# Performance work log

Hardware: AMD Instinct MI355X
Metric: run time of the kernel (lower is better)

Reference implementation:

```python
import jax, jax.numpy as jnp
import numpy as np

N_WORD, N_DOC, E = 20000, 20000, 500000
H, O, D = 4, 32, 128  # heads, out per head, hidden*heads
NEG_SLOPE = 0.2


def setup_inputs() -> dict:
    key = jax.random.key(0)
    ks = jax.random.split(key, 24)
    rn = lambda k, s, sc=0.1: jax.random.normal(k, s, dtype=jnp.float32) * sc
    ri = lambda k, s, hi: jax.random.randint(k, s, 0, hi, dtype=jnp.int32)
    return {
        'x_word': rn(ks[0], (N_WORD, 300), 1.0),
        'x_doc': rn(ks[1], (N_DOC, D), 1.0),
        'Wp_word': rn(ks[2], (300, D)), 'bp_word': jnp.zeros((D,), jnp.float32),
        'Wp_doc': rn(ks[3], (D, D)), 'bp_doc': jnp.zeros((D,), jnp.float32),
        'Wsrc': rn(ks[4], (2, 3, D, D)), 'bsrc': jnp.zeros((2, 3, D), jnp.float32),
        'Wdst': rn(ks[5], (2, 3, D, D)), 'bdst': jnp.zeros((2, 3, D), jnp.float32),
        'attn': rn(ks[6], (2, 3, H, O)), 'bconv': jnp.zeros((2, 3, D), jnp.float32),
        'Wc1': rn(ks[7], (D, 64)), 'bc1': jnp.zeros((64,), jnp.float32),
        'Wc2': rn(ks[8], (64, 64)), 'bc2': jnp.zeros((64,), jnp.float32),
        'src_wd': ri(ks[9], (E,), N_WORD), 'dst_wd': ri(ks[10], (E,), N_DOC),
        'src_dw': ri(ks[11], (E,), N_DOC), 'dst_dw': ri(ks[12], (E,), N_WORD),
        'src_dd': ri(ks[13], (E,), N_DOC), 'dst_dd': ri(ks[14], (E,), N_DOC),
    }


def _gatv2(h_src, h_dst, src, dst, Ws, bs, Wd, bd, a, bias, n_dst):
    # GATv2Conv (DGL): e = a . leaky_relu(Ws h_u + Wd h_v); edge softmax per dst; sum alpha*Ws h_u
    fs = (h_src @ Ws + bs).reshape(-1, H, O)           # [N_src,H,O]
    fd = (h_dst @ Wd + bd).reshape(-1, H, O)           # [N_dst,H,O]
    e = jax.nn.leaky_relu(fs[src] + fd[dst], NEG_SLOPE)  # [E,H,O]
    score = jnp.einsum('eho,ho->eh', e, a)             # [E,H]
    m = jax.lax.stop_gradient(jax.ops.segment_max(score, dst, num_segments=n_dst))
    ex = jnp.exp(score - m[dst])
    s = jax.ops.segment_sum(ex, dst, num_segments=n_dst)
    alpha = ex / s[dst]                                 # per-dst softmax
    rst = jax.ops.segment_sum(alpha[:, :, None] * fs[src], dst, num_segments=n_dst)
    return rst + bias.reshape(1, H, O)


def reference(x_word, x_doc, Wp_word, bp_word, Wp_doc, bp_doc, Wsrc, bsrc, Wdst, bdst,
              attn, bconv, Wc1, bc1, Wc2, bc2, src_wd, dst_wd, src_dw, dst_dw, src_dd, dst_dd):
    h_w = x_word @ Wp_word + bp_word
    h_d = x_doc @ Wp_doc + bp_doc
    for l in range(2):
        o_wd = _gatv2(h_w, h_d, src_wd, dst_wd, Wsrc[l, 0], bsrc[l, 0], Wdst[l, 0], bdst[l, 0], attn[l, 0], bconv[l, 0], N_DOC)
        o_dw = _gatv2(h_d, h_w, src_dw, dst_dw, Wsrc[l, 1], bsrc[l, 1], Wdst[l, 1], bdst[l, 1], attn[l, 1], bconv[l, 1], N_WORD)
        o_dd = _gatv2(h_d, h_d, src_dd, dst_dd, Wsrc[l, 2], bsrc[l, 2], Wdst[l, 2], bdst[l, 2], attn[l, 2], bconv[l, 2], N_DOC)
        h_d = ((o_wd + o_dd) * 0.5).reshape(N_DOC, D)   # mean over 2 relations into 'document'
        h_w = o_dw.reshape(N_WORD, D)                    # mean over 1 relation into 'word'
    z = jax.nn.relu(h_d @ Wc1 + bc1)
    return z @ Wc2 + bc2  # [N_DOC, len_label]
```

## Files before the change

### kernel.cpp

```cpp
#include <hip/hip_runtime.h>

#define NNODE 20000
#define NEDGE 500000
#define CAP 64
#define RCHUNK 2048
#define NRANGE 8
#define RSZ 2500
#define SCAP 70000
#define XW 64

typedef __attribute__((ext_vector_type(8))) short bf16x8;
typedef __attribute__((ext_vector_type(8))) unsigned short u16x8;
typedef __attribute__((ext_vector_type(4))) float f32x4;

__device__ __forceinline__ unsigned short f2bf(float f) {
    unsigned u = __float_as_uint(f);
    return (unsigned short)((u + 0x7FFFu + ((u >> 16) & 1u)) >> 16);
}
__device__ __forceinline__ float bf2f(unsigned short h) {
    return __uint_as_float((unsigned)h << 16);
}

__device__ __forceinline__ void split_one(
    const float* __restrict__ B, unsigned short* __restrict__ Bt,
    int K, int N, int Kp, int i)
{
    int n = i / Kp, k = i % Kp;
    float v = (k < K) ? B[(size_t)k * N + n] : 0.f;
    unsigned short h = f2bf(v);
    Bt[i] = h;
    Bt[(size_t)N * Kp + i] = f2bf(v - bf2f(h));
}

__device__ __forceinline__ void split_row4(
    const float* __restrict__ X, unsigned short* __restrict__ A2,
    int K, int Kp, int r, int c)
{
    float v[4];
#pragma unroll
    for (int j = 0; j < 4; ++j) v[j] = (c + j < K) ? X[(size_t)r * K + c + j] : 0.f;
    ushort4 hi, lo;
    unsigned short h;
    h = f2bf(v[0]); hi.x = h; lo.x = f2bf(v[0] - bf2f(h));
    h = f2bf(v[1]); hi.y = h; lo.y = f2bf(v[1] - bf2f(h));
    h = f2bf(v[2]); hi.z = h; lo.z = f2bf(v[2] - bf2f(h));
    h = f2bf(v[3]); hi.w = h; lo.w = f2bf(v[3] - bf2f(h));
    *reinterpret_cast<ushort4*>(A2 + (size_t)r * 2 * Kp + c) = hi;
    *reinterpret_cast<ushort4*>(A2 + (size_t)r * 2 * Kp + Kp + c) = lo;
}

__global__ __launch_bounds__(256) void prep_all_kernel(
    const float* __restrict__ Wp_word, const float* __restrict__ Wp_doc,
    const float* __restrict__ Wsrc, const float* __restrict__ Wdst,
    const float* __restrict__ Wc1, const float* __restrict__ Wc2,
    const float* __restrict__ xw, const float* __restrict__ xd,
    unsigned short* __restrict__ WtPw, unsigned short* __restrict__ WtPd,
    unsigned short* __restrict__ WtCat,
    unsigned short* __restrict__ WtC1, unsigned short* __restrict__ WtC2,
    unsigned short* __restrict__ Ax, unsigned short* __restrict__ Axd)
{
    int i = blockIdx.x * 256 + threadIdx.x;
    const int S0 = 128 * 320, S1 = 128 * 128, S2 = 6 * 256 * 128;
    const int S3 = 64 * 128, S4 = 64 * 64;
    const int X1 = NNODE * 80, X2 = NNODE * 32;
    if (i < S0) { split_one(Wp_word, WtPw, 300, 128, 320, i); return; }
    i -= S0;
    if (i < S1) { split_one(Wp_doc, WtPd, 128, 128, 128, i); return; }
    i -= S1;
    if (i < S2) {
        int lc = i / (256 * 128), rem = i % (256 * 128);
        int n = rem / 128, k = rem % 128;
        int l = lc / 3, c = lc % 3;
        int half = n >> 7, nn = n & 127;
        const float* M;
        if (c == 0)      M = half ? (Wdst + (size_t)(l * 3 + 1) * 16384) : (Wsrc + (size_t)(l * 3 + 0) * 16384);
        else if (c == 1) M = half ? (Wsrc + (size_t)(l * 3 + 1) * 16384) : (Wdst + (size_t)(l * 3 + 0) * 16384);
        else             M = half ? (Wdst + (size_t)(l * 3 + 2) * 16384) : (Wsrc + (size_t)(l * 3 + 2) * 16384);
        float v = M[(size_t)k * 128 + nn];
        unsigned short h = f2bf(v);
        unsigned short* Bt = WtCat + (size_t)lc * 65536;
        Bt[(size_t)n * 128 + k] = h;
        Bt[32768 + (size_t)n * 128 + k] = f2bf(v - bf2f(h));
        return;
    }
    i -= S2;
    if (i < S3) { split_one(Wc1, WtC1, 128, 64, 128, i); return; }
    i -= S3;
    if (i < S4) { split_one(Wc2, WtC2, 64, 64, 64, i); return; }
    i -= S4;
    if (i < X1) {
        int r = i / 80, c = (i % 80) * 4;
        split_row4(xw, Ax, 300, 320, r, c);
        return;
    }
    i -= X1;
    if (i < X2) {
        int r = i / 32, c = (i % 32) * 4;
        split_row4(xd, Axd, 128, 128, r, c);
    }
}

template<int BM, int BN, int MODE>
__global__ __launch_bounds__(512) void gemm_mfma_kernel(
    const unsigned short* __restrict__ A2,
    const unsigned short* __restrict__ Bt,
    const float* __restrict__ b0,
    float* __restrict__ C0, unsigned short* __restrict__ S0,
    int M, int Kp, int do_relu)
{
    constexpr int FM = BM / 32;
    constexpr int FN = BN / 64;
    __shared__ unsigned short As[2][BM][40];
    __shared__ unsigned short Bs[2][BN][40];
    const int tid = threadIdx.x;
    const int m0 = blockIdx.x * BM;
    const int wid = tid >> 6, lane = tid & 63;
    const int wm = wid >> 2, wn = wid & 3;
    const int lr = lane & 15, kg = lane >> 4;

    f32x4 acc[FM][FN] = {};
    const size_t KA = 2 * (size_t)Kp;
    const size_t PB = (size_t)BN * Kp;

    for (int k0 = 0; k0 < Kp; k0 += 32) {
#pragma unroll
        for (int idx = tid; idx < BM * 4; idx += 512) {
            int row = idx >> 2, ck = idx & 3;
            u16x8 hi = {0,0,0,0,0,0,0,0}, lo = {0,0,0,0,0,0,0,0};
            if (m0 + row < M) {
                const unsigned short* ap = A2 + (size_t)(m0 + row) * KA + k0 + ck * 8;
                hi = *reinterpret_cast<const u16x8*>(ap);
                lo = *reinterpret_cast<const u16x8*>(ap + Kp);
            }
            *reinterpret_cast<u16x8*>(&As[0][row][ck * 8]) = hi;
            *reinterpret_cast<u16x8*>(&As[1][row][ck * 8]) = lo;
        }
#pragma unroll
        for (int idx = tid; idx < BN * 4; idx += 512) {
            int nr = idx >> 2, ck = idx & 3;
            const unsigned short* bp = Bt + (size_t)nr * Kp + k0 + ck * 8;
            *reinterpret_cast<u16x8*>(&Bs[0][nr][ck * 8]) = *reinterpret_cast<const u16x8*>(bp);
            *reinterpret_cast<u16x8*>(&Bs[1][nr][ck * 8]) = *reinterpret_cast<const u16x8*>(bp + PB);
        }
        __syncthreads();
        bf16x8 ah[FM], al[FM], bh[FN], bl[FN];
#pragma unroll
        for (int fm = 0; fm < FM; ++fm) {
            ah[fm] = *reinterpret_cast<const bf16x8*>(&As[0][wm * (BM / 2) + fm * 16 + lr][kg * 8]);
            al[fm] = *reinterpret_cast<const bf16x8*>(&As[1][wm * (BM / 2) + fm * 16 + lr][kg * 8]);
        }
#pragma unroll
        for (int fn = 0; fn < FN; ++fn) {
            bh[fn] = *reinterpret_cast<const bf16x8*>(&Bs[0][wn * (BN / 4) + fn * 16 + lr][kg * 8]);
            bl[fn] = *reinterpret_cast<const bf16x8*>(&Bs[1][wn * (BN / 4) + fn * 16 + lr][kg * 8]);
        }
#pragma unroll
        for (int fm = 0; fm < FM; ++fm)
#pragma unroll
            for (int fn = 0; fn < FN; ++fn) {
                acc[fm][fn] = __builtin_amdgcn_mfma_f32_16x16x32_bf16(ah[fm], bh[fn], acc[fm][fn], 0, 0, 0);
                acc[fm][fn] = __builtin_amdgcn_mfma_f32_16x16x32_bf16(al[fm], bh[fn], acc[fm][fn], 0, 0, 0);
                acc[fm][fn] = __builtin_amdgcn_mfma_f32_16x16x32_bf16(ah[fm], bl[fn], acc[fm][fn], 0, 0, 0);
            }
        __syncthreads();
    }
#pragma unroll
    for (int fm = 0; fm < FM; ++fm)
#pragma unroll
        for (int fn = 0; fn < FN; ++fn) {
            int gc = wn * (BN / 4) + fn * 16 + lr;
            float bv = b0[gc];
#pragma unroll
            for (int j = 0; j < 4; ++j) {
                int gr = m0 + wm * (BM / 2) + fm * 16 + kg * 4 + j;
                if (gr < M) {
                    float v = acc[fm][fn][j] + bv;
                    if (do_relu) v = fmaxf(v, 0.f);
                    if (MODE == 0) {
                        C0[(size_t)gr * BN + gc] = v;
                    } else {
                        unsigned short h = f2bf(v);
                        S0[(size_t)gr * 2 * BN + gc] = h;
                        S0[(size_t)gr * 2 * BN + BN + gc] = f2bf(v - bf2f(h));
                    }
                }
            }
        }
}

struct Cat3Args {
    const unsigned short* A[3];
    const unsigned short* Bt[3];
    const float* bs0[3];
    const float* bs1[3];
    unsigned short* P0[3];
    unsigned short* P1[3];
};

__global__ __launch_bounds__(512) void gemm_cat3_kernel(Cat3Args args, int M)
{
    constexpr int BM = 128, BN = 256, FM = 4, FN = 4, Kp = 128;
    const int y = blockIdx.y;
    const unsigned short* __restrict__ A2 = args.A[y];
    const unsigned short* __restrict__ Bt = args.Bt[y];
    __shared__ unsigned short As[2][BM][40];
    __shared__ unsigned short Bs[2][BN][40];
    const int tid = threadIdx.x;
    const int m0 = blockIdx.x * BM;
    const int wid = tid >> 6, lane = tid & 63;
    const int wm = wid >> 2, wn = wid & 3;
    const int lr = lane & 15, kg = lane >> 4;

    f32x4 acc[FM][FN] = {};
    const size_t KA = 2 * (size_t)Kp;
    const size_t PB = (size_t)BN * Kp;

    for (int k0 = 0; k0 < Kp; k0 += 32) {
#pragma unroll
        for (int idx = tid; idx < BM * 4; idx += 512) {
            int row = idx >> 2, ck = idx & 3;
            u16x8 hi = {0,0,0,0,0,0,0,0}, lo = {0,0,0,0,0,0,0,0};
            if (m0 + row < M) {
                const unsigned short* ap = A2 + (size_t)(m0 + row) * KA + k0 + ck * 8;
                hi = *reinterpret_cast<const u16x8*>(ap);
                lo = *reinterpret_cast<const u16x8*>(ap + Kp);
            }
            *reinterpret_cast<u16x8*>(&As[0][row][ck * 8]) = hi;
            *reinterpret_cast<u16x8*>(&As[1][row][ck * 8]) = lo;
        }
#pragma unroll
        for (int idx = tid; idx < BN * 4; idx += 512) {
            int nr = idx >> 2, ck = idx & 3;
            const unsigned short* bp = Bt + (size_t)nr * Kp + k0 + ck * 8;
            *reinterpret_cast<u16x8*>(&Bs[0][nr][ck * 8]) = *reinterpret_cast<const u16x8*>(bp);
            *reinterpret_cast<u16x8*>(&Bs[1][nr][ck * 8]) = *reinterpret_cast<const u16x8*>(bp + PB);
        }
        __syncthreads();
        bf16x8 ah[FM], al[FM], bh[FN], bl[FN];
#pragma unroll
        for (int fm = 0; fm < FM; ++fm) {
            ah[fm] = *reinterpret_cast<const bf16x8*>(&As[0][wm * 64 + fm * 16 + lr][kg * 8]);
            al[fm] = *reinterpret_cast<const bf16x8*>(&As[1][wm * 64 + fm * 16 + lr][kg * 8]);
        }
#pragma unroll
        for (int fn = 0; fn < FN; ++fn) {
            bh[fn] = *reinterpret_cast<const bf16x8*>(&Bs[0][wn * 64 + fn * 16 + lr][kg * 8]);
            bl[fn] = *reinterpret_cast<const bf16x8*>(&Bs[1][wn * 64 + fn * 16 + lr][kg * 8]);
        }
#pragma unroll
        for (int fm = 0; fm < FM; ++fm)
#pragma unroll
            for (int fn = 0; fn < FN; ++fn) {
                acc[fm][fn] = __builtin_amdgcn_mfma_f32_16x16x32_bf16(ah[fm], bh[fn], acc[fm][fn], 0, 0, 0);
                acc[fm][fn] = __builtin_amdgcn_mfma_f32_16x16x32_bf16(al[fm], bh[fn], acc[fm][fn], 0, 0, 0);
                acc[fm][fn] = __builtin_amdgcn_mfma_f32_16x16x32_bf16(ah[fm], bl[fn], acc[fm][fn], 0, 0, 0);
            }
        __syncthreads();
    }
    const float* __restrict__ bs0 = args.bs0[y];
    const float* __restrict__ bs1 = args.bs1[y];
    unsigned short* __restrict__ P0 = args.P0[y];
    unsigned short* __restrict__ P1 = args.P1[y];
#pragma unroll
    for (int fm = 0; fm < FM; ++fm)
#pragma unroll
        for (int fn = 0; fn < FN; ++fn) {
            int gc = wn * 64 + fn * 16 + lr;
            float bv = (gc < 128) ? bs0[gc] : bs1[gc - 128];
#pragma unroll
            for (int j = 0; j < 4; ++j) {
                int gr = m0 + wm * 64 + fm * 16 + kg * 4 + j;
                if (gr < M) {
                    float v = acc[fm][fn][j] + bv;
                    unsigned short h = f2bf(v);
                    if (gc < 128) P0[(size_t)gr * 128 + gc] = h;
                    else          P1[(size_t)gr * 128 + gc - 128] = h;
                }
            }
        }
}

__global__ __launch_bounds__(256) void route_kernel(
    const int* __restrict__ s0, const int* __restrict__ d0,
    const int* __restrict__ s1, const int* __restrict__ d1,
    const int* __restrict__ s2, const int* __restrict__ d2,
    unsigned* __restrict__ stage, int* __restrict__ scur)
{
    __shared__ unsigned sbuf[RCHUNK];
    __shared__ int hcnt[NRANGE], hoff[NRANGE], gbase[NRANGE], hcur[NRANGE];
    const int rel = blockIdx.y;
    const int c0 = blockIdx.x * RCHUNK;
    const int n = (c0 + RCHUNK <= NEDGE) ? RCHUNK : (NEDGE - c0);
    const int tid = threadIdx.x;
    const int* sp = rel == 0 ? s0 : rel == 1 ? s1 : s2;
    const int* dp = rel == 0 ? d0 : rel == 1 ? d1 : d2;

    if (tid < NRANGE) hcnt[tid] = 0;
    __syncthreads();
    for (int i = tid; i < n; i += 256) atomicAdd(&hcnt[dp[c0 + i] / RSZ], 1);
    __syncthreads();
    if (tid == 0) {
        int o = 0;
        for (int r = 0; r < NRANGE; ++r) {
            hoff[r] = o; hcur[r] = o; o += hcnt[r];
            gbase[r] = atomicAdd(&scur[rel * NRANGE + r], hcnt[r]);
        }
    }
    __syncthreads();
    for (int i = tid; i < n; i += 256) {
        int d = dp[c0 + i], s = sp[c0 + i];
        int k = atomicAdd(&hcur[d / RSZ], 1);
        sbuf[k] = ((unsigned)d << 16) | (unsigned)s;
    }
    __syncthreads();
    for (int r = 0; r < NRANGE; ++r) {
        int cnt = hcnt[r];
        int lim = SCAP - gbase[r];
        if (cnt > lim) cnt = lim;
        unsigned* dst = stage + (size_t)(rel * NRANGE + r) * SCAP + gbase[r];
        for (int i = tid; i < cnt; i += 256) dst[i] = sbuf[hoff[r] + i];
    }
}

__global__ __launch_bounds__(256) void xfill_kernel(
    const unsigned* __restrict__ stage, const int* __restrict__ scur,
    int* __restrict__ deg, unsigned short* __restrict__ csr)
{
    const int r = blockIdx.x & 7;
    const int w = blockIdx.x >> 3;
    const int tid = threadIdx.x;
#pragma unroll
    for (int rel = 0; rel < 3; ++rel) {
        int total = scur[rel * NRANGE + r];
        if (total > SCAP) total = SCAP;
        const unsigned* st = stage + (size_t)(rel * NRANGE + r) * SCAP;
        int* dg = deg + rel * NNODE;
        unsigned short* cb = csr + (size_t)rel * NNODE * CAP;
        for (int i = w * 256 + tid; i < total; i += XW * 256) {
            unsigned p = st[i];
            int d = (int)(p >> 16), s = (int)(p & 0xFFFFu);
            int k = atomicAdd(&dg[d], 1);
            if (k < CAP) cb[(size_t)d * CAP + k] = (unsigned short)s;
        }
    }
}

__device__ __forceinline__ void rel_accum2(
    const unsigned short* __restrict__ fsP,
    const unsigned short* __restrict__ fdP,
    const int* __restrict__ dg, const unsigned short* __restrict__ csrc,
    const float* __restrict__ attnRow,
    int d, int lane, float wscale, float* __restrict__ out)
{
    const int e0 = d * CAP;
    int degv = dg[d];
    if (degv > CAP) degv = CAP;
    const int e1 = e0 + degv;
    float fdv[8], av[8];
    {
        u16x8 t = *reinterpret_cast<const u16x8*>(fdP + (size_t)d * 128 + lane * 8);
#pragma unroll
        for (int j = 0; j < 8; ++j) fdv[j] = bf2f(t[j]);
    }
#pragma unroll
    for (int j = 0; j < 8; ++j) av[j] = attnRow[lane * 8 + j];

    float ssum = 0.f;
    float acc[8];
#pragma unroll
    for (int j = 0; j < 8; ++j) acc[j] = 0.f;

    int i = e0;
    for (; i + 4 <= e1; i += 4) {
        int s0 = csrc[i], s1 = csrc[i + 1], s2 = csrc[i + 2], s3 = csrc[i + 3];
        u16x8 q0 = *reinterpret_cast<const u16x8*>(fsP + (size_t)s0 * 128 + lane * 8);
        u16x8 q1 = *reinterpret_cast<const u16x8*>(fsP + (size_t)s1 * 128 + lane * 8);
        u16x8 q2 = *reinterpret_cast<const u16x8*>(fsP + (size_t)s2 * 128 + lane * 8);
        u16x8 q3 = *reinterpret_cast<const u16x8*>(fsP + (size_t)s3 * 128 + lane * 8);
        float u0[8], u1[8], u2[8], u3[8];
        float pa0 = 0.f, pb0 = 0.f, pa1 = 0.f, pb1 = 0.f;
        float pa2 = 0.f, pb2 = 0.f, pa3 = 0.f, pb3 = 0.f;
#pragma unroll
        for (int j = 0; j < 8; ++j) {
            u0[j] = bf2f(q0[j]); float z = u0[j] + fdv[j];
            pa0 = fmaf(av[j], z, pa0); pb0 = fmaf(av[j], fabsf(z), pb0);
        }
#pragma unroll
        for (int j = 0; j < 8; ++j) {
            u1[j] = bf2f(q1[j]); float z = u1[j] + fdv[j];
            pa1 = fmaf(av[j], z, pa1); pb1 = fmaf(av[j], fabsf(z), pb1);
        }
#pragma unroll
        for (int j = 0; j < 8; ++j) {
            u2[j] = bf2f(q2[j]); float z = u2[j] + fdv[j];
            pa2 = fmaf(av[j], z, pa2); pb2 = fmaf(av[j], fabsf(z), pb2);
        }
#pragma unroll
        for (int j = 0; j < 8; ++j) {
            u3[j] = bf2f(q3[j]); float z = u3[j] + fdv[j];
            pa3 = fmaf(av[j], z, pa3); pb3 = fmaf(av[j], fabsf(z), pb3);
        }
        float p0 = fmaf(0.4f, pb0, 0.6f * pa0);
        float p1 = fmaf(0.4f, pb1, 0.6f * pa1);
        float p2 = fmaf(0.4f, pb2, 0.6f * pa2);
        float p3 = fmaf(0.4f, pb3, 0.6f * pa3);
        p0 += __shfl_xor(p0, 1); p0 += __shfl_xor(p0, 2);
        p1 += __shfl_xor(p1, 1); p1 += __shfl_xor(p1, 2);
        p2 += __shfl_xor(p2, 1); p2 += __shfl_xor(p2, 2);
        p3 += __shfl_xor(p3, 1); p3 += __shfl_xor(p3, 2);
        float w0 = __expf(p0), w1 = __expf(p1);
        float w2 = __expf(p2), w3 = __expf(p3);
        ssum += (w0 + w1) + (w2 + w3);
#pragma unroll
        for (int j = 0; j < 8; ++j)
            acc[j] += fmaf(w0, u0[j], w1 * u1[j]) + fmaf(w2, u2[j], w3 * u3[j]);
    }
    for (; i < e1; ++i) {
        int s0 = csrc[i];
        u16x8 q0 = *reinterpret_cast<const u16x8*>(fsP + (size_t)s0 * 128 + lane * 8);
        float u0[8];
        float pa = 0.f, pb = 0.f;
#pragma unroll
        for (int j = 0; j < 8; ++j) {
            u0[j] = bf2f(q0[j]); float z = u0[j] + fdv[j];
            pa = fmaf(av[j], z, pa); pb = fmaf(av[j], fabsf(z), pb);
        }
        float p0 = fmaf(0.4f, pb, 0.6f * pa);
        p0 += __shfl_xor(p0, 1); p0 += __shfl_xor(p0, 2);
        float w = __expf(p0);
        ssum += w;
#pragma unroll
        for (int j = 0; j < 8; ++j) acc[j] = fmaf(w, u0[j], acc[j]);
    }
    float inv = (ssum > 0.f) ? wscale / ssum : 0.f;
#pragma unroll
    for (int j = 0; j < 8; ++j) out[j] += inv * acc[j];
}

struct ConvJob {
    const unsigned short *fsA, *fdA;
    const int* degA; const unsigned short* csrA;
    const float *attnA, *biasA;
    const unsigned short *fsB, *fdB;
    const int* degB; const unsigned short* csrB;
    const float *attnB, *biasB;
    float wscale;
    unsigned short* sp;
};

__global__ __launch_bounds__(256) void gat_conv2_kernel(
    ConvJob J0, ConvJob J1, int nblk0)
{
    const bool first = ((int)blockIdx.x < nblk0);
    const ConvJob J = first ? J0 : J1;
    const int b = first ? blockIdx.x : blockIdx.x - nblk0;
    int gid = b * 256 + threadIdx.x;
    int d = gid >> 4, lane = gid & 15;
    if (d >= NNODE) return;
    float out[8];
#pragma unroll
    for (int j = 0; j < 8; ++j) {
        float bb = J.biasA[lane * 8 + j];
        if (J.biasB) bb += J.biasB[lane * 8 + j];
        out[j] = J.wscale * bb;
    }
    rel_accum2(J.fsA, J.fdA, J.degA, J.csrA, J.attnA, d, lane, J.wscale, out);
    if (J.fsB)
        rel_accum2(J.fsB, J.fdB, J.degB, J.csrB, J.attnB, d, lane, J.wscale, out);
    u16x8 hv, lv;
#pragma unroll
    for (int j = 0; j < 8; ++j) {
        unsigned short h = f2bf(out[j]);
        hv[j] = h;
        lv[j] = f2bf(out[j] - bf2f(h));
    }
    *reinterpret_cast<u16x8*>(J.sp + (size_t)d * 256 + lane * 8) = hv;
    *reinterpret_cast<u16x8*>(J.sp + (size_t)d * 256 + 128 + lane * 8) = lv;
}

extern "C" void kernel_launch(void* const* d_in, const int* in_sizes, int n_in,
                              void* d_out, int out_size, void* d_ws, size_t ws_size,
                              hipStream_t stream)
{
    const float* x_word  = (const float*)d_in[0];
    const float* x_doc   = (const float*)d_in[1];
    const float* Wp_word = (const float*)d_in[2];
    const float* bp_word = (const float*)d_in[3];
    const float* Wp_doc  = (const float*)d_in[4];
    const float* bp_doc  = (const float*)d_in[5];
    const float* Wsrc    = (const float*)d_in[6];
    const float* bsrc    = (const float*)d_in[7];
    const float* Wdst    = (const float*)d_in[8];
    const float* bdst    = (const float*)d_in[9];
    const float* attn    = (const float*)d_in[10];
    const float* bconv   = (const float*)d_in[11];
    const float* Wc1     = (const float*)d_in[12];
    const float* bc1     = (const float*)d_in[13];
    const float* Wc2     = (const float*)d_in[14];
    const float* bc2     = (const float*)d_in[15];
    const int* src_wd = (const int*)d_in[16];
    const int* dst_wd = (const int*)d_in[17];
    const int* src_dw = (const int*)d_in[18];
    const int* dst_dw = (const int*)d_in[19];
    const int* src_dd = (const int*)d_in[20];
    const int* dst_dd = (const int*)d_in[21];

    const size_t NP = (size_t)NNODE * 128;
    unsigned short* U = (unsigned short*)d_ws;
    unsigned short* Pfs_wd = U;
    unsigned short* Pfd_dw = U + 1 * NP;
    unsigned short* Pfd_wd = U + 2 * NP;
    unsigned short* Pfs_dw = U + 3 * NP;
    unsigned short* Pfs_dd = U + 4 * NP;
    unsigned short* Pfd_dd = U + 5 * NP;
    unsigned short* AswA = U + 6 * NP;
    unsigned short* AsdA = AswA + 2 * NP;
    unsigned short* AswB = AsdA + 2 * NP;
    unsigned short* AsdB = AswB + 2 * NP;
    unsigned short* WtPw  = AsdB + 2 * NP;
    unsigned short* WtPd  = WtPw + 81920;
    unsigned short* WtCat = WtPd + 32768;
    unsigned short* WtC1  = WtCat + 393216;
    unsigned short* WtC2  = WtC1 + 16384;
    unsigned short* Ax  = Pfs_wd;
    unsigned short* Axd = AswB;
    unsigned short* Az  = AswB;
    int* I    = (int*)(WtC2 + 8192);
    int* deg  = I;
    int* scur = I + 3 * NNODE;
    unsigned* stage = (unsigned*)(scur + 32);
    unsigned short* csrp = (unsigned short*)(stage + 3 * NRANGE * SCAP);

    const int GB128 = (NNODE + 127) / 128;
    const int CB = (NNODE * 16 + 255) / 256;
    const int RB = (NEDGE + RCHUNK - 1) / RCHUNK;

    (void)hipMemsetAsync(deg, 0, (3 * NNODE + 32) * sizeof(int), stream);
    route_kernel<<<dim3(RB, 3), 256, 0, stream>>>(
        src_wd, dst_wd, src_dw, dst_dw, src_dd, dst_dd, stage, scur);
    xfill_kernel<<<NRANGE * XW, 256, 0, stream>>>(stage, scur, deg, csrp);

    const int PREP = 266240 + NNODE * 112;
    prep_all_kernel<<<(PREP + 255) / 256, 256, 0, stream>>>(
        Wp_word, Wp_doc, Wsrc, Wdst, Wc1, Wc2, x_word, x_doc,
        WtPw, WtPd, WtCat, WtC1, WtC2, Ax, Axd);

    gemm_mfma_kernel<128, 128, 2><<<GB128, 512, 0, stream>>>(
        Ax, WtPw, bp_word, nullptr, AswA, NNODE, 320, 0);
    gemm_mfma_kernel<128, 128, 2><<<GB128, 512, 0, stream>>>(
        Axd, WtPd, bp_doc, nullptr, AsdA, NNODE, 128, 0);

    const unsigned short* Asw_in = AswA;
    const unsigned short* Asd_in = AsdA;
    for (int l = 0; l < 2; ++l) {
        const int l3 = l * 3;
        Cat3Args ca;
        ca.A[0] = Asw_in; ca.A[1] = Asd_in; ca.A[2] = Asd_in;
        ca.Bt[0] = WtCat + (size_t)(l3 + 0) * 65536;
        ca.Bt[1] = WtCat + (size_t)(l3 + 1) * 65536;
        ca.Bt[2] = WtCat + (size_t)(l3 + 2) * 65536;
        ca.bs0[0] = bsrc + (l3 + 0) * 128; ca.bs1[0] = bdst + (l3 + 1) * 128;
        ca.bs0[1] = bdst + (l3 + 0) * 128; ca.bs1[1] = bsrc + (l3 + 1) * 128;
        ca.bs0[2] = bsrc + (l3 + 2) * 128; ca.bs1[2] = bdst + (l3 + 2) * 128;
        ca.P0[0] = Pfs_wd; ca.P1[0] = Pfd_dw;
        ca.P0[1] = Pfd_wd; ca.P1[1] = Pfs_dw;
        ca.P0[2] = Pfs_dd; ca.P1[2] = Pfd_dd;
        gemm_cat3_kernel<<<dim3(GB128, 3), 512, 0, stream>>>(ca, NNODE);

        ConvJob jd;
        jd.fsA = Pfs_wd; jd.fdA = Pfd_wd; jd.degA = deg;             jd.csrA = csrp;
        jd.attnA = attn + (l3 + 0) * 128; jd.biasA = bconv + (l3 + 0) * 128;
        jd.fsB = Pfs_dd; jd.fdB = Pfd_dd; jd.degB = deg + 2 * NNODE; jd.csrB = csrp + (size_t)2 * NNODE * CAP;
        jd.attnB = attn + (l3 + 2) * 128; jd.biasB = bconv + (l3 + 2) * 128;
        jd.wscale = 0.5f; jd.sp = (l == 0 ? AsdB : AsdA);

        if (l == 0) {
            ConvJob jw;
            jw.fsA = Pfs_dw; jw.fdA = Pfd_dw; jw.degA = deg + NNODE; jw.csrA = csrp + (size_t)NNODE * CAP;
            jw.attnA = attn + (l3 + 1) * 128; jw.biasA = bconv + (l3 + 1) * 128;
            jw.fsB = nullptr; jw.fdB = nullptr; jw.degB = nullptr; jw.csrB = nullptr;
            jw.attnB = nullptr; jw.biasB = nullptr;
            jw.wscale = 1.0f; jw.sp = AswB;
            gat_conv2_kernel<<<2 * CB, 256, 0, stream>>>(jd, jw, CB);
        } else {
            gat_conv2_kernel<<<CB, 256, 0, stream>>>(jd, jd, CB);
        }
        Asw_in = AswB;
        Asd_in = AsdB;
    }

    gemm_mfma_kernel<128, 64, 2><<<GB128, 512, 0, stream>>>(
        AsdA, WtC1, bc1, nullptr, Az, NNODE, 128, 1);
    gemm_mfma_kernel<128, 64, 0><<<GB128, 512, 0, stream>>>(
        Az, WtC2, bc2, (float*)d_out, nullptr, NNODE, 64, 0);
}
```

Before: 379.1 us.

## Split per-destination GAT aggregation across two half-waves for more parallelism

Each destination node now uses 32 threads instead of 16. For doc nodes the two halves process the two relations (word→doc and doc→doc) concurrently. For word nodes the two halves split the edge list, and partial softmax sums and accumulators are combined with cross-lane shuffles. This doubles the thread count and shortens the serial edge loop per thread, which should expose more memory-level parallelism for the gathers. The cost is extra shuffles, and half the threads sit idle during the final store.

After: 370.6 us. 2.3% less time.

```diff
diff --git a/kernel.cpp b/kernel.cpp
--- a/kernel.cpp
+++ b/kernel.cpp
@@ -345,17 +345,14 @@
     }
 }
 
-__device__ __forceinline__ void rel_accum2(
+__device__ __forceinline__ void rel_raw(
     const unsigned short* __restrict__ fsP,
     const unsigned short* __restrict__ fdP,
-    const int* __restrict__ dg, const unsigned short* __restrict__ csrc,
+    const unsigned short* __restrict__ csrc,
     const float* __restrict__ attnRow,
-    int d, int lane, float wscale, float* __restrict__ out)
-{
-    const int e0 = d * CAP;
-    int degv = dg[d];
-    if (degv > CAP) degv = CAP;
-    const int e1 = e0 + degv;
+    int d, int lane, int iBeg, int iEnd,
+    float& ssum, float* __restrict__ acc)
+{
     float fdv[8], av[8];
     {
         u16x8 t = *reinterpret_cast<const u16x8*>(fdP + (size_t)d * 128 + lane * 8);
@@ -365,13 +362,8 @@
 #pragma unroll
     for (int j = 0; j < 8; ++j) av[j] = attnRow[lane * 8 + j];
 
-    float ssum = 0.f;
-    float acc[8];
-#pragma unroll
-    for (int j = 0; j < 8; ++j) acc[j] = 0.f;
-
-    int i = e0;
-    for (; i + 4 <= e1; i += 4) {
+    int i = iBeg;
+    for (; i + 4 <= iEnd; i += 4) {
         int s0 = csrc[i], s1 = csrc[i + 1], s2 = csrc[i + 2], s3 = csrc[i + 3];
         u16x8 q0 = *reinterpret_cast<const u16x8*>(fsP + (size_t)s0 * 128 + lane * 8);
         u16x8 q1 = *reinterpret_cast<const u16x8*>(fsP + (size_t)s1 * 128 + lane * 8);
@@ -415,7 +407,7 @@
         for (int j = 0; j < 8; ++j)
             acc[j] += fmaf(w0, u0[j], w1 * u1[j]) + fmaf(w2, u2[j], w3 * u3[j]);
     }
-    for (; i < e1; ++i) {
+    for (; i < iEnd; ++i) {
         int s0 = csrc[i];
         u16x8 q0 = *reinterpret_cast<const u16x8*>(fsP + (size_t)s0 * 128 + lane * 8);
         float u0[8];
@@ -432,9 +424,6 @@
 #pragma unroll
         for (int j = 0; j < 8; ++j) acc[j] = fmaf(w, u0[j], acc[j]);
     }
-    float inv = (ssum > 0.f) ? wscale / ssum : 0.f;
-#pragma unroll
-    for (int j = 0; j < 8; ++j) out[j] += inv * acc[j];
 }
 
 struct ConvJob {
@@ -448,34 +437,66 @@
     unsigned short* sp;
 };
 
-__global__ __launch_bounds__(256) void gat_conv2_kernel(
+__global__ __launch_bounds__(256) void gat_conv3_kernel(
     ConvJob J0, ConvJob J1, int nblk0)
 {
     const bool first = ((int)blockIdx.x < nblk0);
     const ConvJob J = first ? J0 : J1;
-    const int b = first ? blockIdx.x : blockIdx.x - nblk0;
+    const int b = first ? (int)blockIdx.x : (int)blockIdx.x - nblk0;
     int gid = b * 256 + threadIdx.x;
-    int d = gid >> 4, lane = gid & 15;
+    int d = gid >> 5;
+    int lane = gid & 15;
+    int half = (gid >> 4) & 1;
     if (d >= NNODE) return;
-    float out[8];
-#pragma unroll
-    for (int j = 0; j < 8; ++j) {
-        float bb = J.biasA[lane * 8 + j];
-        if (J.biasB) bb += J.biasB[lane * 8 + j];
-        out[j] = J.wscale * bb;
-    }
-    rel_accum2(J.fsA, J.fdA, J.degA, J.csrA, J.attnA, d, lane, J.wscale, out);
-    if (J.fsB)
-        rel_accum2(J.fsB, J.fdB, J.degB, J.csrB, J.attnB, d, lane, J.wscale, out);
-    u16x8 hv, lv;
-#pragma unroll
-    for (int j = 0; j < 8; ++j) {
-        unsigned short h = f2bf(out[j]);
-        hv[j] = h;
-        lv[j] = f2bf(out[j] - bf2f(h));
-    }
-    *reinterpret_cast<u16x8*>(J.sp + (size_t)d * 256 + lane * 8) = hv;
-    *reinterpret_cast<u16x8*>(J.sp + (size_t)d * 256 + 128 + lane * 8) = lv;
+
+    float ssum = 0.f;
+    float acc[8];
+#pragma unroll
+    for (int j = 0; j < 8; ++j) acc[j] = 0.f;
+    float r[8];
+
+    if (J.fsB) {
+        const unsigned short* fs = half ? J.fsB : J.fsA;
+        const unsigned short* fd = half ? J.fdB : J.fdA;
+        const int* dgp           = half ? J.degB : J.degA;
+        const unsigned short* cs = half ? J.csrB : J.csrA;
+        const float* at          = half ? J.attnB : J.attnA;
+        int deg = dgp[d]; if (deg > CAP) deg = CAP;
+        rel_raw(fs, fd, cs, at, d, lane, d * CAP, d * CAP + deg, ssum, acc);
+        float inv = (ssum > 0.f) ? J.wscale / ssum : 0.f;
+#pragma unroll
+        for (int j = 0; j < 8; ++j) {
+            r[j] = inv * acc[j];
+            r[j] += __shfl_xor(r[j], 16);
+        }
+    } else {
+        int deg = J.degA[d]; if (deg > CAP) deg = CAP;
+        int h = (deg + 1) >> 1;
+        int iB = d * CAP + (half ? h : 0);
+        int iE = d * CAP + (half ? deg : h);
+        rel_raw(J.fsA, J.fdA, J.csrA, J.attnA, d, lane, iB, iE, ssum, acc);
+        ssum += __shfl_xor(ssum, 16);
+#pragma unroll
+        for (int j = 0; j < 8; ++j) acc[j] += __shfl_xor(acc[j], 16);
+        float inv = (ssum > 0.f) ? J.wscale / ssum : 0.f;
+#pragma unroll
+        for (int j = 0; j < 8; ++j) r[j] = inv * acc[j];
+    }
+
+    if (half == 0) {
+        u16x8 hv, lv;
+#pragma unroll
+        for (int j = 0; j < 8; ++j) {
+            float bb = J.biasA[lane * 8 + j];
+            if (J.biasB) bb += J.biasB[lane * 8 + j];
+            float o = J.wscale * bb + r[j];
+            unsigned short hh = f2bf(o);
+            hv[j] = hh;
+            lv[j] = f2bf(o - bf2f(hh));
+        }
+        *reinterpret_cast<u16x8*>(J.sp + (size_t)d * 256 + lane * 8) = hv;
+        *reinterpret_cast<u16x8*>(J.sp + (size_t)d * 256 + 128 + lane * 8) = lv;
+    }
 }
 
 extern "C" void kernel_launch(void* const* d_in, const int* in_sizes, int n_in,
@@ -532,7 +553,7 @@
     unsigned short* csrp = (unsigned short*)(stage + 3 * NRANGE * SCAP);
 
     const int GB128 = (NNODE + 127) / 128;
-    const int CB = (NNODE * 16 + 255) / 256;
+    const int CB32 = (NNODE * 32) / 256;
     const int RB = (NEDGE + RCHUNK - 1) / RCHUNK;
 
     (void)hipMemsetAsync(deg, 0, (3 * NNODE + 32) * sizeof(int), stream);
@@ -581,9 +602,9 @@
             jw.fsB = nullptr; jw.fdB = nullptr; jw.degB = nullptr; jw.csrB = nullptr;
             jw.attnB = nullptr; jw.biasB = nullptr;
             jw.wscale = 1.0f; jw.sp = AswB;
-            gat_conv2_kernel<<<2 * CB, 256, 0, stream>>>(jd, jw, CB);
+            gat_conv3_kernel<<<2 * CB32, 256, 0, stream>>>(jd, jw, CB32);
         } else {
-            gat_conv2_kernel<<<CB, 256, 0, stream>>>(jd, jd, CB);
+            gat_conv3_kernel<<<CB32, 256, 0, stream>>>(jd, jd, CB32);
         }
         Asw_in = AswB;
         Asd_in = AsdB;
```
